# Optimization experiments

Measured on AMD Instinct MI355X. Metric: run time of the kernel, lower is better.

## Reference

```python
import jax, jax.numpy as jnp
import numpy as np

B, T, C = 4, 2048, 1024
H, D = 16, 64          # n_head, head_size; H*D == C
FF = 4 * C             # compute_layer_scaling * n_embed
EPS = 1e-5


def layernorm(x, g, b):
    mu = jnp.mean(x, axis=-1, keepdims=True)
    var = jnp.var(x, axis=-1, keepdims=True)
    return (x - mu) * jax.lax.rsqrt(var + EPS) * g + b


def setup_inputs() -> dict:
    key = jax.random.key(0)
    ks = jax.random.split(key, 12)
    s_c = 1.0 / np.sqrt(C)
    s_ff = 1.0 / np.sqrt(FF)
    return {
        "x": jax.random.normal(ks[0], (B, T, C), dtype=jnp.float32),
        # per-head Q/K/V weights, stacked: [H, C, D] (Linear with bias=False)
        "Wq": jax.random.normal(ks[1], (H, C, D), dtype=jnp.float32) * s_c,
        "Wk": jax.random.normal(ks[2], (H, C, D), dtype=jnp.float32) * s_c,
        "Wv": jax.random.normal(ks[3], (H, C, D), dtype=jnp.float32) * s_c,
        "Wproj": jax.random.normal(ks[4], (C, C), dtype=jnp.float32) * s_c,
        "bproj": jnp.zeros((C,), dtype=jnp.float32),
        "W1": jax.random.normal(ks[5], (C, FF), dtype=jnp.float32) * s_c,
        "b1": jnp.zeros((FF,), dtype=jnp.float32),
        "W2": jax.random.normal(ks[6], (FF, FF), dtype=jnp.float32) * s_ff,
        "b2": jnp.zeros((FF,), dtype=jnp.float32),
        "W3": jax.random.normal(ks[7], (FF, C), dtype=jnp.float32) * s_ff,
        "b3": jnp.zeros((C,), dtype=jnp.float32),
        "ln1_g": jnp.ones((C,), dtype=jnp.float32),
        "ln1_b": jnp.zeros((C,), dtype=jnp.float32),
        "ln2_g": jnp.ones((C,), dtype=jnp.float32),
        "ln2_b": jnp.zeros((C,), dtype=jnp.float32),
    }


def reference(x, Wq, Wk, Wv, Wproj, bproj, W1, b1, W2, b2, W3, b3,
              ln1_g, ln1_b, ln2_g, ln2_b):
    # --- multi-head causal self-attention (pre-LN) ---
    h = layernorm(x, ln1_g, ln1_b)
    q = jnp.einsum("btc,hcd->bhtd", h, Wq)
    k = jnp.einsum("btc,hcd->bhtd", h, Wk)
    v = jnp.einsum("btc,hcd->bhtd", h, Wv)
    # NOTE: original scales by n_embed**-0.5 (C from x.shape), not head_size
    scores = jnp.einsum("bhtd,bhsd->bhts", q, k) * (C ** -0.5)
    causal = jnp.tril(jnp.ones((T, T), dtype=bool))
    scores = jnp.where(causal, scores, -jnp.inf)
    wei = jax.nn.softmax(scores, axis=-1)          # dropout p=0 -> identity
    attn = jnp.einsum("bhts,bhsd->bhtd", wei, v)
    attn = attn.transpose(0, 2, 1, 3).reshape(B, T, C)  # concat heads
    x = x + attn @ Wproj + bproj
    # --- feed-forward (pre-LN): C -> FF -> relu -> FF -> relu -> C ---
    h2 = layernorm(x, ln2_g, ln2_b)
    h2 = jax.nn.relu(h2 @ W1 + b1)
    h2 = jax.nn.relu(h2 @ W2 + b2)
    x = x + h2 @ W3 + b3
    return x
```

## Files before the change

### kernel.cpp

```cpp
#include <hip/hip_runtime.h>

typedef __bf16 bf16;
typedef bf16  bf16x8 __attribute__((ext_vector_type(8)));
typedef bf16  bf16x4 __attribute__((ext_vector_type(4)));
typedef float f32x4  __attribute__((ext_vector_type(4)));

#define T_SEQ 2048

__device__ __forceinline__ void gload_lds16(const bf16* g, bf16* l) {
    __builtin_amdgcn_global_load_lds(
        (const __attribute__((address_space(1))) unsigned int*)g,
        (__attribute__((address_space(3))) unsigned int*)l,
        16, 0, 0);
}

#define VMCNT(n) asm volatile("s_waitcnt vmcnt(" #n ")" ::: "memory")
#define BAR() do { asm volatile("" ::: "memory"); __builtin_amdgcn_s_barrier(); \
                   asm volatile("" ::: "memory"); } while (0)

__global__ __launch_bounds__(256) void transpose_f32_bf16(
    const float* __restrict__ in, bf16* __restrict__ out, int R, int Cc, int ldo)
{
    __shared__ float tile[32][33];
    const int bx = blockIdx.x * 32;
    const int by = blockIdx.y * 32;
    const long bi = (long)blockIdx.z * R * Cc;
    const long bo = (long)blockIdx.z * Cc * ldo;
    const int tx = threadIdx.x, ty = threadIdx.y;
#pragma unroll
    for (int i = 0; i < 4; ++i)
        tile[ty + i * 8][tx] = in[bi + (long)(by + ty + i * 8) * Cc + bx + tx];
    __syncthreads();
#pragma unroll
    for (int i = 0; i < 4; ++i)
        out[bo + (long)(bx + ty + i * 8) * ldo + by + tx] = (bf16)tile[tx][ty + i * 8];
}

__global__ __launch_bounds__(256) void transpose_bf16(
    const bf16* __restrict__ in, bf16* __restrict__ out, int ldi, int ldo)
{
    __shared__ bf16 tile[32][33];
    const int bx = blockIdx.x * 32;
    const int by = blockIdx.y * 32;
    const int tx = threadIdx.x, ty = threadIdx.y;
#pragma unroll
    for (int i = 0; i < 4; ++i)
        tile[ty + i * 8][tx] = in[(long)(by + ty + i * 8) * ldi + bx + tx];
    __syncthreads();
#pragma unroll
    for (int i = 0; i < 4; ++i)
        out[(long)(bx + ty + i * 8) * ldo + by + tx] = tile[tx][ty + i * 8];
}

__global__ __launch_bounds__(256) void ln_kernel(
    const float* __restrict__ x, const float* __restrict__ g,
    const float* __restrict__ bb, bf16* __restrict__ out)
{
    const long row = blockIdx.x;
    const int tid = threadIdx.x;
    const float4 v = ((const float4*)(x + row * 1024))[tid];
    float s  = v.x + v.y + v.z + v.w;
    float s2 = v.x * v.x + v.y * v.y + v.z * v.z + v.w * v.w;
#pragma unroll
    for (int off = 32; off >= 1; off >>= 1) {
        s  += __shfl_xor(s,  off, 64);
        s2 += __shfl_xor(s2, off, 64);
    }
    __shared__ float red[8];
    const int wid = tid >> 6;
    if ((tid & 63) == 0) { red[wid] = s; red[4 + wid] = s2; }
    __syncthreads();
    s  = red[0] + red[1] + red[2] + red[3];
    s2 = red[4] + red[5] + red[6] + red[7];
    const float mu   = s * (1.f / 1024.f);
    const float rstd = rsqrtf(s2 * (1.f / 1024.f) - mu * mu + 1e-5f);
    const float4 gv = ((const float4*)g)[tid];
    const float4 bv = ((const float4*)bb)[tid];
    bf16x4 ov;
    ov[0] = (bf16)((v.x - mu) * rstd * gv.x + bv.x);
    ov[1] = (bf16)((v.y - mu) * rstd * gv.y + bv.y);
    ov[2] = (bf16)((v.z - mu) * rstd * gv.z + bv.z);
    ov[3] = (bf16)((v.w - mu) * rstd * gv.w + bv.w);
    *(bf16x4*)(out + row * 1024 + tid * 4) = ov;
}

#define LOADA(BUFP, QM) do {                                                   \
    const char* ab_ = (BUFP) + (size_t)((wr * 64 + (QM) * 128 + fr) * 128);    \
    _Pragma("unroll") for (int m_ = 0; m_ < 4; ++m_) {                         \
        af[m_][0] = *(const bf16x8*)(ab_ + m_ * 2048 + so0);                   \
        af[m_][1] = *(const bf16x8*)(ab_ + m_ * 2048 + so1); } } while (0)

#define LOADB(BUFP, QN, DST) do {                                              \
    const char* bb_ = (BUFP) + (size_t)((wc * 32 + (QN) * 128 + fr) * 128);    \
    _Pragma("unroll") for (int n_ = 0; n_ < 2; ++n_) {                         \
        DST[n_][0] = *(const bf16x8*)(bb_ + n_ * 2048 + so0);                  \
        DST[n_][1] = *(const bf16x8*)(bb_ + n_ * 2048 + so1); } } while (0)

#define MMA(ACC, BSET) do { __builtin_amdgcn_s_setprio(1);                     \
    _Pragma("unroll") for (int m_ = 0; m_ < 4; ++m_)                           \
    _Pragma("unroll") for (int n_ = 0; n_ < 2; ++n_) {                         \
        ACC[m_][n_] = __builtin_amdgcn_mfma_f32_16x16x32_bf16(                 \
            af[m_][0], BSET[n_][0], ACC[m_][n_], 0, 0, 0);                     \
        ACC[m_][n_] = __builtin_amdgcn_mfma_f32_16x16x32_bf16(                 \
            af[m_][1], BSET[n_][1], ACC[m_][n_], 0, 0, 0); }                   \
    __builtin_amdgcn_s_setprio(0); } while (0)

#define TB_DEEP(W1N, W3N, ISSN, ISSC) do {                                     \
    const char* abuf = cAs + ((size_t)cur << 15);                              \
    const char* bbuf = cBs + ((size_t)cur << 15);                              \
    const long kb  = (long)(k + 1) * 64;                                       \
    const long kb2 = (long)(k + 2) * 64;                                       \
    LOADA(abuf, 0);                                                            \
    LOADB(bbuf, 0, bfv0);                                                      \
    if (ISSN) stageB(nxt, 0, kb);                                 \
    BAR(); MMA(a00, bfv0); BAR();                                              \
    LOADB(bbuf, 1, bfv1);                                                      \
    if (ISSN) stageA(nxt, 1, kb);                                 \
    VMCNT(W1N);                                                                \
    BAR(); MMA(a01, bfv1); BAR();                                              \
    LOADA(abuf, 1);                                                            \
    if (ISSC) stageA(cur, 0, kb2);                                \
    BAR(); MMA(a11, bfv1); BAR();                                              \
    if (ISSC) stageB(cur, 1, kb2);                                \
    VMCNT(W3N);                                                                \
    BAR(); MMA(a10, bfv0); BAR(); } while (0)

template <int MODE>
__global__ __launch_bounds__(512, 1) void gemm256(
    const bf16* __restrict__ A, const bf16* __restrict__ Bt,
    const float* __restrict__ bias, const float* __restrict__ resid,
    void* __restrict__ outp, int M, int N, int K, int nbn)
{
    extern __shared__ __align__(16) char smem[];
    char* cAs = smem;
    char* cBs = smem + 65536;

    const int tid = threadIdx.x;
    const int wid = tid >> 6, lane = tid & 63;
    const int wr = wid >> 2, wc = wid & 3;
    const int fr = lane & 15, fq = lane >> 4;

    const int nwg = gridDim.x;
    const int cpx = nwg >> 3;
    const int b0  = blockIdx.x;
    const int bid = (b0 & 7) * cpx + (b0 >> 3);
    const long bm = bid / nbn, bn = bid % nbn;
    const long bmrow = bm * 256, bnrow = bn * 256;

    const int srow0 = wid * 8 + (lane >> 3);
    const int sslot = (lane & 7) ^ (lane >> 3);
    auto stageA = [&](int buf, int h, long kt) {
        const bf16* g = A + (size_t)(bmrow + h * 128 + srow0) * K + kt + sslot * 8;
        char* l = cAs + ((size_t)buf << 15) + h * 16384 + (size_t)wid * 1024;
        gload_lds16(g, (bf16*)l);
        gload_lds16(g + (size_t)64 * K, (bf16*)(l + 8192));
    };
    auto stageB = [&](int buf, int h, long kt) {
        const bf16* g = Bt + (size_t)(bnrow + h * 128 + srow0) * K + kt + sslot * 8;
        char* l = cBs + ((size_t)buf << 15) + h * 16384 + (size_t)wid * 1024;
        gload_lds16(g, (bf16*)l);
        gload_lds16(g + (size_t)64 * K, (bf16*)(l + 8192));
    };

    const int sx  = fr & 7;
    const int so0 = ((fq) ^ sx) * 16;
    const int so1 = ((4 + fq) ^ sx) * 16;

    bf16x8 af[4][2], bfv0[2][2], bfv1[2][2];
    f32x4 a00[4][2], a01[4][2], a11[4][2], a10[4][2];
#pragma unroll
    for (int m = 0; m < 4; ++m)
#pragma unroll
        for (int n = 0; n < 2; ++n) {
            a00[m][n] = {0.f, 0.f, 0.f, 0.f}; a01[m][n] = {0.f, 0.f, 0.f, 0.f};
            a11[m][n] = {0.f, 0.f, 0.f, 0.f}; a10[m][n] = {0.f, 0.f, 0.f, 0.f};
        }

    stageA(0, 0, 0);
    stageB(0, 1, 0);
    stageB(0, 0, 0);
    stageA(0, 1, 0);
    stageA(1, 0, 64);
    stageB(1, 1, 64);
    VMCNT(6);
    BAR();

    const int NT = K >> 6;
    int cur, nxt;
    int k = 0;
    for (; k < NT - 2; ++k) {
        cur = k & 1; nxt = cur ^ 1;
        TB_DEEP(8, 6, true, true);
    }
    cur = k & 1; nxt = cur ^ 1;
    TB_DEEP(8, 2, true, false);
    ++k;
    cur = k & 1; nxt = cur ^ 1;
    TB_DEEP(0, 0, false, false);

    auto writeQ = [&](f32x4 (&acc)[4][2], int QM, int QN) {
#pragma unroll
        for (int m = 0; m < 4; ++m) {
            const long row0 = bmrow + wr * 64 + QM * 128 + m * 16 + fq * 4;
#pragma unroll
            for (int n = 0; n < 2; ++n) {
                const long col = bnrow + wc * 32 + QN * 128 + n * 16 + fr;
                const float bv = (MODE == 0) ? 0.f : bias[col];
#pragma unroll
                for (int j = 0; j < 4; ++j) {
                    const long row = row0 + j;
                    float v = acc[m][n][j] + bv;
                    if (MODE == 1) v = fmaxf(v, 0.f);
                    if (MODE == 2) {
                        v += resid[row * N + col];
                        ((float*)outp)[row * N + col] = v;
                    } else {
                        ((bf16*)outp)[row * N + col] = (bf16)v;
                    }
                }
            }
        }
    };
    writeQ(a00, 0, 0); writeQ(a01, 0, 1); writeQ(a11, 1, 1); writeQ(a10, 1, 0);
}

#define TILE_BODY_N(PRE, LAST) do {                                            \
    const char* abuf = cAs + ((size_t)cur << 15);                              \
    const char* bbuf = cBs + ((size_t)cur << 14);                              \
    const long kn = (long)(k + 1) * 64;                                        \
    LOADA(abuf, 0);                                                            \
    LOADB(bbuf, 0, bfv);                                                       \
    if (PRE) { stageA(nxt, 0, kn); stageB(nxt, kn); stageA(nxt, 1, kn);        \
               VMCNT(6); }                                                     \
    else     { VMCNT(0); }                                                     \
    BAR(); MMA(aq0, bfv); BAR();                                               \
    LOADA(abuf, 1);                                                            \
    if (PRE) { VMCNT(2); }                                                     \
    if (!LAST) { BAR(); }                                                      \
    MMA(aq1, bfv);                                                             \
    if (!LAST) { BAR(); } } while (0)

template <int MODE>
__global__ __launch_bounds__(512, 2) void gemm256n(
    const bf16* __restrict__ A, const bf16* __restrict__ Bt,
    const float* __restrict__ bias, const float* __restrict__ resid,
    void* __restrict__ outp, int M, int N, int K, int nbn)
{
    extern __shared__ __align__(16) char smem[];
    char* cAs = smem;
    char* cBs = smem + 65536;

    const int tid = threadIdx.x;
    const int wid = tid >> 6, lane = tid & 63;
    const int wr = wid >> 2, wc = wid & 3;
    const int fr = lane & 15, fq = lane >> 4;

    const int nwg = gridDim.x;
    const int cpx = nwg >> 3;
    const int b0  = blockIdx.x;
    const int bid = (b0 & 7) * cpx + (b0 >> 3);
    const long bm = bid / nbn, bn = bid % nbn;
    const long bmrow = bm * 256, bnrow = bn * 128;

    const int srow0 = wid * 8 + (lane >> 3);
    const int sslot = (lane & 7) ^ (lane >> 3);
    auto stageA = [&](int buf, int h, long kt) {
        const bf16* g = A + (size_t)(bmrow + h * 128 + srow0) * K + kt + sslot * 8;
        char* l = cAs + ((size_t)buf << 15) + h * 16384 + (size_t)wid * 1024;
        gload_lds16(g, (bf16*)l);
        gload_lds16(g + (size_t)64 * K, (bf16*)(l + 8192));
    };
    auto stageB = [&](int buf, long kt) {
        const bf16* g = Bt + (size_t)(bnrow + srow0) * K + kt + sslot * 8;
        char* l = cBs + ((size_t)buf << 14) + (size_t)wid * 1024;
        gload_lds16(g, (bf16*)l);
        gload_lds16(g + (size_t)64 * K, (bf16*)(l + 8192));
    };

    const int sx  = fr & 7;
    const int so0 = ((fq) ^ sx) * 16;
    const int so1 = ((4 + fq) ^ sx) * 16;

    bf16x8 af[4][2], bfv[2][2];
    f32x4 aq0[4][2], aq1[4][2];
#pragma unroll
    for (int m = 0; m < 4; ++m)
#pragma unroll
        for (int n = 0; n < 2; ++n) {
            aq0[m][n] = {0.f, 0.f, 0.f, 0.f};
            aq1[m][n] = {0.f, 0.f, 0.f, 0.f};
        }

    stageA(0, 0, 0); stageB(0, 0); stageA(0, 1, 0);
    VMCNT(2);
    BAR();

    const int NT = K >> 6;
    int cur = 0, nxt = 1;
    int k = 0;
    for (; k < NT - 1; ++k) {
        cur = k & 1; nxt = cur ^ 1;
        TILE_BODY_N(true, false);
    }
    cur = k & 1; nxt = cur ^ 1;
    TILE_BODY_N(false, true);

    auto writeQ = [&](f32x4 (&acc)[4][2], int QM) {
#pragma unroll
        for (int m = 0; m < 4; ++m) {
            const long row0 = bmrow + wr * 64 + QM * 128 + m * 16 + fq * 4;
#pragma unroll
            for (int n = 0; n < 2; ++n) {
                const long col = bnrow + wc * 32 + n * 16 + fr;
                const float bv = (MODE == 0) ? 0.f : bias[col];
#pragma unroll
                for (int j = 0; j < 4; ++j) {
                    const long row = row0 + j;
                    float v = acc[m][n][j] + bv;
                    if (MODE == 1) v = fmaxf(v, 0.f);
                    if (MODE == 2) {
                        v += resid[row * N + col];
                        ((float*)outp)[row * N + col] = v;
                    } else {
                        ((bf16*)outp)[row * N + col] = (bf16)v;
                    }
                }
            }
        }
    };
    writeQ(aq0, 0); writeQ(aq1, 1);
}

__device__ __forceinline__ void attn_step(
    const bf16* __restrict__ Ks, const bf16* __restrict__ Vt,
    bf16* __restrict__ Pp, const bf16x8* qf,
    f32x4* o, f32x4& o_l, float* mj, const bf16x8 onesf,
    int fr, int fq, int qloc, bool diag)
{
    f32x4 s[4];
#pragma unroll
    for (int n = 0; n < 4; ++n) s[n] = {0.f, 0.f, 0.f, 0.f};
#pragma unroll
    for (int n = 0; n < 4; ++n) {
        const int t  = n * 16 + fr;
        const int sw = ((t ^ (t >> 3)) & 7) << 4;
#pragma unroll
        for (int kk = 0; kk < 2; ++kk) {
            const bf16x8 kf = *(const bf16x8*)((const char*)Ks + t * 128
                                               + ((kk * 64 + fq * 16) ^ sw));
            s[n] = __builtin_amdgcn_mfma_f32_16x16x32_bf16(qf[kk], kf, s[n], 0, 0, 0);
        }
    }
    float v[4][4], mxj[4];
#pragma unroll
    for (int j = 0; j < 4; ++j) {
        const int qg = qloc + fq * 4 + j;
        v[0][j] = s[0][j] * 0.03125f;
        v[1][j] = s[1][j] * 0.03125f;
        v[2][j] = s[2][j] * 0.03125f;
        v[3][j] = s[3][j] * 0.03125f;
        if (diag) {
            if (fr      > qg) v[0][j] = -1e30f;
            if (16 + fr > qg) v[1][j] = -1e30f;
            if (32 + fr > qg) v[2][j] = -1e30f;
            if (48 + fr > qg) v[3][j] = -1e30f;
        }
        float mx = fmaxf(fmaxf(v[0][j], v[1][j]), fmaxf(v[2][j], v[3][j]));
#pragma unroll
        for (int off = 1; off <= 8; off <<= 1) mx = fmaxf(mx, __shfl_xor(mx, off, 16));
        mxj[j] = mx;
    }
    float need = mxj[0] - mj[0];
    need = fmaxf(need, mxj[1] - mj[1]);
    need = fmaxf(need, mxj[2] - mj[2]);
    need = fmaxf(need, mxj[3] - mj[3]);
    if (__any(need > 8.f)) {
#pragma unroll
        for (int j = 0; j < 4; ++j) {
            const float mn   = fmaxf(mj[j], mxj[j]);
            const float corr = __expf(mj[j] - mn);
            mj[j] = mn;
#pragma unroll
            for (int nd = 0; nd < 4; ++nd) o[nd][j] *= corr;
            o_l[j] *= corr;
        }
    }
#pragma unroll
    for (int j = 0; j < 4; ++j) {
        bf16* prow = Pp + (fq * 4 + j) * 72;
        prow[fr]      = (bf16)__expf(v[0][j] - mj[j]);
        prow[16 + fr] = (bf16)__expf(v[1][j] - mj[j]);
        prow[32 + fr] = (bf16)__expf(v[2][j] - mj[j]);
        prow[48 + fr] = (bf16)__expf(v[3][j] - mj[j]);
    }
    asm volatile("s_waitcnt lgkmcnt(0)" ::: "memory");
    __builtin_amdgcn_sched_barrier(0);
    const bf16x8 pf0 = *(const bf16x8*)(Pp + fr * 72 + fq * 8);
    const bf16x8 pf1 = *(const bf16x8*)(Pp + fr * 72 + 32 + fq * 8);
#pragma unroll
    for (int nd = 0; nd < 4; ++nd) {
        const int dd = nd * 16 + fr;
        const int sw = ((dd ^ (dd >> 3)) & 7) << 4;
        const bf16x8 vf0 = *(const bf16x8*)((const char*)Vt + dd * 128 + ((fq * 16) ^ sw));
        const bf16x8 vf1 = *(const bf16x8*)((const char*)Vt + dd * 128 + ((64 + fq * 16) ^ sw));
        o[nd] = __builtin_amdgcn_mfma_f32_16x16x32_bf16(pf0, vf0, o[nd], 0, 0, 0);
        o[nd] = __builtin_amdgcn_mfma_f32_16x16x32_bf16(pf1, vf1, o[nd], 0, 0, 0);
    }
    o_l = __builtin_amdgcn_mfma_f32_16x16x32_bf16(pf0, onesf, o_l, 0, 0, 0);
    o_l = __builtin_amdgcn_mfma_f32_16x16x32_bf16(pf1, onesf, o_l, 0, 0, 0);
}

__global__ __launch_bounds__(256) void attn_kernel(
    const bf16* __restrict__ qkv, const bf16* __restrict__ vt,
    bf16* __restrict__ out)
{
    const int pair = blockIdx.x;
    const int h = blockIdx.y, b = blockIdx.z;
    const int tid = threadIdx.x, wid = tid >> 6, lane = tid & 63;
    const int fr = lane & 15, fq = lane >> 4;
    const int jA = pair, jB = 31 - pair;
    const bf16* baseQ = qkv + ((long)b * T_SEQ) * 3072 + h * 64;
    const bf16* baseK = baseQ + 1024;
    const bf16* baseV = vt + (long)(h * 64) * 8192 + (long)b * T_SEQ;

    __shared__ __align__(16) bf16 Ks[2][64 * 64];
    __shared__ __align__(16) bf16 Vs[2][64 * 64];
    __shared__ __align__(16) bf16 Plds[4][16 * 72];

    const int qrA = jA * 64 + wid * 16 + fr;
    const int qrB = jB * 64 + wid * 16 + fr;
    bf16x8 qfA[2], qfB[2];
#pragma unroll
    for (int kk = 0; kk < 2; ++kk) {
        qfA[kk] = *(const bf16x8*)(baseQ + (long)qrA * 3072 + kk * 32 + fq * 8);
        qfB[kk] = *(const bf16x8*)(baseQ + (long)qrB * 3072 + kk * 32 + fq * 8);
    }

    bf16x8 onesf;
    {
        const bf16 ov = (fr == 0) ? (bf16)1.f : (bf16)0.f;
#pragma unroll
        for (int e = 0; e < 8; ++e) onesf[e] = ov;
    }

    f32x4 oA[4], oB[4], olA, olB;
    float mA[4], mB[4];
#pragma unroll
    for (int nd = 0; nd < 4; ++nd) { oA[nd] = {0.f, 0.f, 0.f, 0.f}; oB[nd] = {0.f, 0.f, 0.f, 0.f}; }
    olA = {0.f, 0.f, 0.f, 0.f}; olB = {0.f, 0.f, 0.f, 0.f};
#pragma unroll
    for (int j = 0; j < 4; ++j) { mA[j] = -1e30f; mB[j] = -1e30f; }

    const int t_p0 = wid * 16 + (lane >> 3);
    const int t_p1 = t_p0 + 8;
    const int kcb0 = ((lane & 7) * 16) ^ (((t_p0 ^ (t_p0 >> 3)) & 7) << 4);
    const int kcb1 = ((lane & 7) * 16) ^ (((t_p1 ^ (t_p1 >> 3)) & 7) << 4);

    bf16* P = &Plds[wid][0];

    auto stage = [&](int buf, int c) {
        const long s0 = (long)c * 64;
        gload_lds16(baseK + (s0 + t_p0) * 3072 + (kcb0 >> 1), &Ks[buf][(wid * 2) * 512]);
        gload_lds16(baseK + (s0 + t_p1) * 3072 + (kcb1 >> 1), &Ks[buf][(wid * 2 + 1) * 512]);
        gload_lds16(baseV + (long)t_p0 * 8192 + s0 + (kcb0 >> 1), &Vs[buf][(wid * 2) * 512]);
        gload_lds16(baseV + (long)t_p1 * 8192 + s0 + (kcb1 >> 1), &Vs[buf][(wid * 2 + 1) * 512]);
    };

    const int nch = jB + 1;
    stage(0, 0);
    for (int c = 0; c < nch; ++c) {
        const int cur = c & 1;
        if (c + 1 < nch) { stage(cur ^ 1, c + 1); VMCNT(4); }
        else             { VMCNT(0); }
        BAR();
        if (c <= jA)
            attn_step(Ks[cur], Vs[cur], P, qfA, oA, olA, mA, onesf, fr, fq, wid * 16, c == jA);
        attn_step(Ks[cur], Vs[cur], P, qfB, oB, olB, mB, onesf, fr, fq, wid * 16, c == jB);
        BAR();
    }

#pragma unroll
    for (int j = 0; j < 4; ++j) {
        const float lA = __shfl(olA[j], lane & 48, 64);
        const float lB = __shfl(olB[j], lane & 48, 64);
        const float rA = 1.f / lA, rB = 1.f / lB;
        const long rowA = (long)b * T_SEQ + jA * 64 + wid * 16 + fq * 4 + j;
        const long rowB = (long)b * T_SEQ + jB * 64 + wid * 16 + fq * 4 + j;
#pragma unroll
        for (int nd = 0; nd < 4; ++nd) {
            out[rowA * 1024 + h * 64 + nd * 16 + fr] = (bf16)(oA[nd][j] * rA);
            out[rowB * 1024 + h * 64 + nd * 16 + fr] = (bf16)(oB[nd][j] * rB);
        }
    }
}

extern "C" void kernel_launch(void* const* d_in, const int* in_sizes, int n_in,
                              void* d_out, int out_size, void* d_ws, size_t ws_size,
                              hipStream_t stream)
{
    const float* x     = (const float*)d_in[0];
    const float* Wq    = (const float*)d_in[1];
    const float* Wk    = (const float*)d_in[2];
    const float* Wv    = (const float*)d_in[3];
    const float* Wproj = (const float*)d_in[4];
    const float* bproj = (const float*)d_in[5];
    const float* W1    = (const float*)d_in[6];
    const float* b1    = (const float*)d_in[7];
    const float* W2    = (const float*)d_in[8];
    const float* b2    = (const float*)d_in[9];
    const float* W3    = (const float*)d_in[10];
    const float* b3    = (const float*)d_in[11];
    const float* ln1g  = (const float*)d_in[12];
    const float* ln1b  = (const float*)d_in[13];
    const float* ln2g  = (const float*)d_in[14];
    const float* ln2b  = (const float*)d_in[15];

    char* ws = (char*)d_ws;
    size_t off = 0;
    auto alloc = [&](size_t bytes) {
        void* p = ws + off;
        off += (bytes + 255) & ~(size_t)255;
        return p;
    };
    bf16* Wqkv_t  = (bf16*)alloc(3072ul * 1024 * 2);
    bf16* Wproj_t = (bf16*)alloc(1024ul * 1024 * 2);
    bf16* W1_t    = (bf16*)alloc(4096ul * 1024 * 2);
    bf16* W2_t    = (bf16*)alloc(4096ul * 4096 * 2);
    bf16* W3_t    = (bf16*)alloc(1024ul * 4096 * 2);
    bf16* hbuf    = (bf16*)alloc(8192ul * 1024 * 2);
    float* x1     = (float*)alloc(8192ul * 1024 * 4);
    bf16* a1      = (bf16*)alloc(8192ul * 4096 * 2);
    char* R1      = (char*)alloc(8192ul * 4096 * 2);
    bf16* qkvb    = (bf16*)R1;
    bf16* attnb   = (bf16*)(R1 + 8192ul * 3072 * 2);
    bf16* a2      = (bf16*)R1;
    bf16* vt      = a1;

    hipFuncSetAttribute(reinterpret_cast<const void*>(&gemm256<1>),
                        hipFuncAttributeMaxDynamicSharedMemorySize, 131072);
    hipFuncSetAttribute(reinterpret_cast<const void*>(&gemm256n<0>),
                        hipFuncAttributeMaxDynamicSharedMemorySize, 98304);
    hipFuncSetAttribute(reinterpret_cast<const void*>(&gemm256n<2>),
                        hipFuncAttributeMaxDynamicSharedMemorySize, 98304);

    const dim3 tb(32, 8);
    transpose_f32_bf16<<<dim3(2, 32, 16), tb, 0, stream>>>(Wq, Wqkv_t,                1024, 64, 1024);
    transpose_f32_bf16<<<dim3(2, 32, 16), tb, 0, stream>>>(Wk, Wqkv_t + 1024l * 1024, 1024, 64, 1024);
    transpose_f32_bf16<<<dim3(2, 32, 16), tb, 0, stream>>>(Wv, Wqkv_t + 2048l * 1024, 1024, 64, 1024);
    transpose_f32_bf16<<<dim3(32, 32, 1),   tb, 0, stream>>>(Wproj, Wproj_t, 1024, 1024, 1024);
    transpose_f32_bf16<<<dim3(128, 32, 1),  tb, 0, stream>>>(W1, W1_t, 1024, 4096, 1024);
    transpose_f32_bf16<<<dim3(128, 128, 1), tb, 0, stream>>>(W2, W2_t, 4096, 4096, 4096);
    transpose_f32_bf16<<<dim3(32, 128, 1),  tb, 0, stream>>>(W3, W3_t, 4096, 1024, 4096);

    ln_kernel<<<8192, 256, 0, stream>>>(x, ln1g, ln1b, hbuf);
    gemm256n<0><<<768, 512, 98304, stream>>>(hbuf, Wqkv_t, nullptr, nullptr, qkvb,
                                             8192, 3072, 1024, 24);
    transpose_bf16<<<dim3(32, 256), tb, 0, stream>>>(qkvb + 2048, vt, 3072, 8192);
    attn_kernel<<<dim3(16, 16, 4), 256, 0, stream>>>(qkvb, vt, attnb);
    gemm256n<2><<<256, 512, 98304, stream>>>(attnb, Wproj_t, bproj, x, x1,
                                             8192, 1024, 1024, 8);
    ln_kernel<<<8192, 256, 0, stream>>>(x1, ln2g, ln2b, hbuf);
    gemm256<1><<<512, 512, 131072, stream>>>(hbuf, W1_t, b1, nullptr, a1,
                                             8192, 4096, 1024, 16);
    gemm256<1><<<512, 512, 131072, stream>>>(a1, W2_t, b2, nullptr, a2,
                                             8192, 4096, 4096, 16);
    gemm256n<2><<<256, 512, 98304, stream>>>(a2, W3_t, b3, x1, (float*)d_out,
                                             8192, 1024, 4096, 8);
}
```

Before: 677.5 us.

## Share K/V fragment loads across paired query tiles and store residual in bf16

The attention inner step now handles both query tiles (A and B) in one fused step. It loads each K and V fragment from LDS once and issues MFMAs for both tiles, using a separate P buffer per tile and raising wave priority around the MFMA blocks. The intermediate residual x1 is stored in bf16 instead of fp32, with a new bf16-input layernorm and new GEMM epilogue modes. This cuts LDS reads in attention and global traffic for the residual, at the cost of more register pressure and slightly lower residual precision.

```diff
diff --git a/kernel.cpp b/kernel.cpp
--- a/kernel.cpp
+++ b/kernel.cpp
@@ -81,6 +81,40 @@
     ov[1] = (bf16)((v.y - mu) * rstd * gv.y + bv.y);
     ov[2] = (bf16)((v.z - mu) * rstd * gv.z + bv.z);
     ov[3] = (bf16)((v.w - mu) * rstd * gv.w + bv.w);
+    *(bf16x4*)(out + row * 1024 + tid * 4) = ov;
+}
+
+__global__ __launch_bounds__(256) void ln_kernel_b(
+    const bf16* __restrict__ x, const float* __restrict__ g,
+    const float* __restrict__ bb, bf16* __restrict__ out)
+{
+    const long row = blockIdx.x;
+    const int tid = threadIdx.x;
+    const bf16x4 vb = ((const bf16x4*)(x + row * 1024))[tid];
+    const float v0 = (float)vb[0], v1 = (float)vb[1];
+    const float v2 = (float)vb[2], v3 = (float)vb[3];
+    float s  = v0 + v1 + v2 + v3;
+    float s2 = v0 * v0 + v1 * v1 + v2 * v2 + v3 * v3;
+#pragma unroll
+    for (int off = 32; off >= 1; off >>= 1) {
+        s  += __shfl_xor(s,  off, 64);
+        s2 += __shfl_xor(s2, off, 64);
+    }
+    __shared__ float red[8];
+    const int wid = tid >> 6;
+    if ((tid & 63) == 0) { red[wid] = s; red[4 + wid] = s2; }
+    __syncthreads();
+    s  = red[0] + red[1] + red[2] + red[3];
+    s2 = red[4] + red[5] + red[6] + red[7];
+    const float mu   = s * (1.f / 1024.f);
+    const float rstd = rsqrtf(s2 * (1.f / 1024.f) - mu * mu + 1e-5f);
+    const float4 gv = ((const float4*)g)[tid];
+    const float4 bv = ((const float4*)bb)[tid];
+    bf16x4 ov;
+    ov[0] = (bf16)((v0 - mu) * rstd * gv.x + bv.x);
+    ov[1] = (bf16)((v1 - mu) * rstd * gv.y + bv.y);
+    ov[2] = (bf16)((v2 - mu) * rstd * gv.z + bv.z);
+    ov[3] = (bf16)((v3 - mu) * rstd * gv.w + bv.w);
     *(bf16x4*)(out + row * 1024 + tid * 4) = ov;
 }
 
@@ -243,7 +277,7 @@
 template <int MODE>
 __global__ __launch_bounds__(512, 2) void gemm256n(
     const bf16* __restrict__ A, const bf16* __restrict__ Bt,
-    const float* __restrict__ bias, const float* __restrict__ resid,
+    const float* __restrict__ bias, const void* __restrict__ resid,
     void* __restrict__ outp, int M, int N, int K, int nbn)
 {
     extern __shared__ __align__(16) char smem[];
@@ -317,9 +351,11 @@
                 for (int j = 0; j < 4; ++j) {
                     const long row = row0 + j;
                     float v = acc[m][n][j] + bv;
-                    if (MODE == 1) v = fmaxf(v, 0.f);
-                    if (MODE == 2) {
-                        v += resid[row * N + col];
+                    if (MODE == 3) {
+                        v += ((const float*)resid)[row * N + col];
+                        ((bf16*)outp)[row * N + col] = (bf16)v;
+                    } else if (MODE == 4) {
+                        v += (float)((const bf16*)resid)[row * N + col];
                         ((float*)outp)[row * N + col] = v;
                     } else {
                         ((bf16*)outp)[row * N + col] = (bf16)v;
@@ -331,26 +367,10 @@
     writeQ(aq0, 0); writeQ(aq1, 1);
 }
 
-__device__ __forceinline__ void attn_step(
-    const bf16* __restrict__ Ks, const bf16* __restrict__ Vt,
-    bf16* __restrict__ Pp, const bf16x8* qf,
-    f32x4* o, f32x4& o_l, float* mj, const bf16x8 onesf,
+__device__ __forceinline__ void sm_part(
+    f32x4* s, float* mj, f32x4* o, f32x4& o_l, bf16* Pp,
     int fr, int fq, int qloc, bool diag)
 {
-    f32x4 s[4];
-#pragma unroll
-    for (int n = 0; n < 4; ++n) s[n] = {0.f, 0.f, 0.f, 0.f};
-#pragma unroll
-    for (int n = 0; n < 4; ++n) {
-        const int t  = n * 16 + fr;
-        const int sw = ((t ^ (t >> 3)) & 7) << 4;
-#pragma unroll
-        for (int kk = 0; kk < 2; ++kk) {
-            const bf16x8 kf = *(const bf16x8*)((const char*)Ks + t * 128
-                                               + ((kk * 64 + fq * 16) ^ sw));
-            s[n] = __builtin_amdgcn_mfma_f32_16x16x32_bf16(qf[kk], kf, s[n], 0, 0, 0);
-        }
-    }
     float v[4][4], mxj[4];
 #pragma unroll
     for (int j = 0; j < 4; ++j) {
@@ -370,10 +390,8 @@
         for (int off = 1; off <= 8; off <<= 1) mx = fmaxf(mx, __shfl_xor(mx, off, 16));
         mxj[j] = mx;
     }
-    float need = mxj[0] - mj[0];
-    need = fmaxf(need, mxj[1] - mj[1]);
-    need = fmaxf(need, mxj[2] - mj[2]);
-    need = fmaxf(need, mxj[3] - mj[3]);
+    float need = fmaxf(fmaxf(mxj[0] - mj[0], mxj[1] - mj[1]),
+                       fmaxf(mxj[2] - mj[2], mxj[3] - mj[3]));
     if (__any(need > 8.f)) {
 #pragma unroll
         for (int j = 0; j < 4; ++j) {
@@ -393,10 +411,34 @@
         prow[32 + fr] = (bf16)__expf(v[2][j] - mj[j]);
         prow[48 + fr] = (bf16)__expf(v[3][j] - mj[j]);
     }
+}
+
+__device__ __forceinline__ void attn_step(
+    const bf16* __restrict__ Ks, const bf16* __restrict__ Vt,
+    bf16* __restrict__ Pp, const bf16x8* qf,
+    f32x4* o, f32x4& o_l, float* mj, const bf16x8 onesf,
+    int fr, int fq, int qloc, bool diag)
+{
+    f32x4 s[4];
+#pragma unroll
+    for (int n = 0; n < 4; ++n) s[n] = {0.f, 0.f, 0.f, 0.f};
+    __builtin_amdgcn_s_setprio(1);
+#pragma unroll
+    for (int n = 0; n < 4; ++n) {
+        const int t  = n * 16 + fr;
+        const int sw = ((t ^ (t >> 3)) & 7) << 4;
+        const bf16x8 kf0 = *(const bf16x8*)((const char*)Ks + t * 128 + ((fq * 16) ^ sw));
+        const bf16x8 kf1 = *(const bf16x8*)((const char*)Ks + t * 128 + ((64 + fq * 16) ^ sw));
+        s[n] = __builtin_amdgcn_mfma_f32_16x16x32_bf16(qf[0], kf0, s[n], 0, 0, 0);
+        s[n] = __builtin_amdgcn_mfma_f32_16x16x32_bf16(qf[1], kf1, s[n], 0, 0, 0);
+    }
+    __builtin_amdgcn_s_setprio(0);
+    sm_part(s, mj, o, o_l, Pp, fr, fq, qloc, diag);
     asm volatile("s_waitcnt lgkmcnt(0)" ::: "memory");
     __builtin_amdgcn_sched_barrier(0);
     const bf16x8 pf0 = *(const bf16x8*)(Pp + fr * 72 + fq * 8);
     const bf16x8 pf1 = *(const bf16x8*)(Pp + fr * 72 + 32 + fq * 8);
+    __builtin_amdgcn_s_setprio(1);
 #pragma unroll
     for (int nd = 0; nd < 4; ++nd) {
         const int dd = nd * 16 + fr;
@@ -408,6 +450,58 @@
     }
     o_l = __builtin_amdgcn_mfma_f32_16x16x32_bf16(pf0, onesf, o_l, 0, 0, 0);
     o_l = __builtin_amdgcn_mfma_f32_16x16x32_bf16(pf1, onesf, o_l, 0, 0, 0);
+    __builtin_amdgcn_s_setprio(0);
+}
+
+__device__ __forceinline__ void attn_step2(
+    const bf16* __restrict__ Ks, const bf16* __restrict__ Vt,
+    bf16* __restrict__ PpA, bf16* __restrict__ PpB,
+    const bf16x8* qfA, const bf16x8* qfB,
+    f32x4* oA, f32x4& olA, float* mA,
+    f32x4* oB, f32x4& olB, float* mB,
+    const bf16x8 onesf, int fr, int fq, int qloc, bool diagA)
+{
+    f32x4 sA[4], sB[4];
+#pragma unroll
+    for (int n = 0; n < 4; ++n) { sA[n] = {0.f, 0.f, 0.f, 0.f}; sB[n] = {0.f, 0.f, 0.f, 0.f}; }
+    __builtin_amdgcn_s_setprio(1);
+#pragma unroll
+    for (int n = 0; n < 4; ++n) {
+        const int t  = n * 16 + fr;
+        const int sw = ((t ^ (t >> 3)) & 7) << 4;
+        const bf16x8 kf0 = *(const bf16x8*)((const char*)Ks + t * 128 + ((fq * 16) ^ sw));
+        const bf16x8 kf1 = *(const bf16x8*)((const char*)Ks + t * 128 + ((64 + fq * 16) ^ sw));
+        sA[n] = __builtin_amdgcn_mfma_f32_16x16x32_bf16(qfA[0], kf0, sA[n], 0, 0, 0);
+        sA[n] = __builtin_amdgcn_mfma_f32_16x16x32_bf16(qfA[1], kf1, sA[n], 0, 0, 0);
+        sB[n] = __builtin_amdgcn_mfma_f32_16x16x32_bf16(qfB[0], kf0, sB[n], 0, 0, 0);
+        sB[n] = __builtin_amdgcn_mfma_f32_16x16x32_bf16(qfB[1], kf1, sB[n], 0, 0, 0);
+    }
+    __builtin_amdgcn_s_setprio(0);
+    sm_part(sA, mA, oA, olA, PpA, fr, fq, qloc, diagA);
+    sm_part(sB, mB, oB, olB, PpB, fr, fq, qloc, false);
+    asm volatile("s_waitcnt lgkmcnt(0)" ::: "memory");
+    __builtin_amdgcn_sched_barrier(0);
+    const bf16x8 pfA0 = *(const bf16x8*)(PpA + fr * 72 + fq * 8);
+    const bf16x8 pfA1 = *(const bf16x8*)(PpA + fr * 72 + 32 + fq * 8);
+    const bf16x8 pfB0 = *(const bf16x8*)(PpB + fr * 72 + fq * 8);
+    const bf16x8 pfB1 = *(const bf16x8*)(PpB + fr * 72 + 32 + fq * 8);
+    __builtin_amdgcn_s_setprio(1);
+#pragma unroll
+    for (int nd = 0; nd < 4; ++nd) {
+        const int dd = nd * 16 + fr;
+        const int sw = ((dd ^ (dd >> 3)) & 7) << 4;
+        const bf16x8 vf0 = *(const bf16x8*)((const char*)Vt + dd * 128 + ((fq * 16) ^ sw));
+        const bf16x8 vf1 = *(const bf16x8*)((const char*)Vt + dd * 128 + ((64 + fq * 16) ^ sw));
+        oA[nd] = __builtin_amdgcn_mfma_f32_16x16x32_bf16(pfA0, vf0, oA[nd], 0, 0, 0);
+        oA[nd] = __builtin_amdgcn_mfma_f32_16x16x32_bf16(pfA1, vf1, oA[nd], 0, 0, 0);
+        oB[nd] = __builtin_amdgcn_mfma_f32_16x16x32_bf16(pfB0, vf0, oB[nd], 0, 0, 0);
+        oB[nd] = __builtin_amdgcn_mfma_f32_16x16x32_bf16(pfB1, vf1, oB[nd], 0, 0, 0);
+    }
+    olA = __builtin_amdgcn_mfma_f32_16x16x32_bf16(pfA0, onesf, olA, 0, 0, 0);
+    olA = __builtin_amdgcn_mfma_f32_16x16x32_bf16(pfA1, onesf, olA, 0, 0, 0);
+    olB = __builtin_amdgcn_mfma_f32_16x16x32_bf16(pfB0, onesf, olB, 0, 0, 0);
+    olB = __builtin_amdgcn_mfma_f32_16x16x32_bf16(pfB1, onesf, olB, 0, 0, 0);
+    __builtin_amdgcn_s_setprio(0);
 }
 
 __global__ __launch_bounds__(256) void attn_kernel(
@@ -425,7 +519,7 @@
 
     __shared__ __align__(16) bf16 Ks[2][64 * 64];
     __shared__ __align__(16) bf16 Vs[2][64 * 64];
-    __shared__ __align__(16) bf16 Plds[4][16 * 72];
+    __shared__ __align__(16) bf16 Plds[2][4][16 * 72];
 
     const int qrA = jA * 64 + wid * 16 + fr;
     const int qrB = jB * 64 + wid * 16 + fr;
@@ -456,7 +550,8 @@
     const int kcb0 = ((lane & 7) * 16) ^ (((t_p0 ^ (t_p0 >> 3)) & 7) << 4);
     const int kcb1 = ((lane & 7) * 16) ^ (((t_p1 ^ (t_p1 >> 3)) & 7) << 4);
 
-    bf16* P = &Plds[wid][0];
+    bf16* PA = &Plds[0][wid][0];
+    bf16* PB = &Plds[1][wid][0];
 
     auto stage = [&](int buf, int c) {
         const long s0 = (long)c * 64;
@@ -474,8 +569,11 @@
         else             { VMCNT(0); }
         BAR();
         if (c <= jA)
-            attn_step(Ks[cur], Vs[cur], P, qfA, oA, olA, mA, onesf, fr, fq, wid * 16, c == jA);
-        attn_step(Ks[cur], Vs[cur], P, qfB, oB, olB, mB, onesf, fr, fq, wid * 16, c == jB);
+            attn_step2(Ks[cur], Vs[cur], PA, PB, qfA, qfB,
+                       oA, olA, mA, oB, olB, mB, onesf, fr, fq, wid * 16, c == jA);
+        else
+            attn_step(Ks[cur], Vs[cur], PB, qfB, oB, olB, mB, onesf,
+                      fr, fq, wid * 16, c == jB);
         BAR();
     }
 
@@ -528,7 +626,7 @@
     bf16* W2_t    = (bf16*)alloc(4096ul * 4096 * 2);
     bf16* W3_t    = (bf16*)alloc(1024ul * 4096 * 2);
     bf16* hbuf    = (bf16*)alloc(8192ul * 1024 * 2);
-    float* x1     = (float*)alloc(8192ul * 1024 * 4);
+    bf16* x1b     = (bf16*)alloc(8192ul * 1024 * 2);
     bf16* a1      = (bf16*)alloc(8192ul * 4096 * 2);
     char* R1      = (char*)alloc(8192ul * 4096 * 2);
     bf16* qkvb    = (bf16*)R1;
@@ -540,7 +638,9 @@
                         hipFuncAttributeMaxDynamicSharedMemorySize, 131072);
     hipFuncSetAttribute(reinterpret_cast<const void*>(&gemm256n<0>),
                         hipFuncAttributeMaxDynamicSharedMemorySize, 98304);
-    hipFuncSetAttribute(reinterpret_cast<const void*>(&gemm256n<2>),
+    hipFuncSetAttribute(reinterpret_cast<const void*>(&gemm256n<3>),
+                        hipFuncAttributeMaxDynamicSharedMemorySize, 98304);
+    hipFuncSetAttribute(reinterpret_cast<const void*>(&gemm256n<4>),
                         hipFuncAttributeMaxDynamicSharedMemorySize, 98304);
 
     const dim3 tb(32, 8);
@@ -557,13 +657,13 @@
                                              8192, 3072, 1024, 24);
     transpose_bf16<<<dim3(32, 256), tb, 0, stream>>>(qkvb + 2048, vt, 3072, 8192);
     attn_kernel<<<dim3(16, 16, 4), 256, 0, stream>>>(qkvb, vt, attnb);
-    gemm256n<2><<<256, 512, 98304, stream>>>(attnb, Wproj_t, bproj, x, x1,
+    gemm256n<3><<<256, 512, 98304, stream>>>(attnb, Wproj_t, bproj, x, x1b,
                                              8192, 1024, 1024, 8);
-    ln_kernel<<<8192, 256, 0, stream>>>(x1, ln2g, ln2b, hbuf);
+    ln_kernel_b<<<8192, 256, 0, stream>>>(x1b, ln2g, ln2b, hbuf);
     gemm256<1><<<512, 512, 131072, stream>>>(hbuf, W1_t, b1, nullptr, a1,
                                              8192, 4096, 1024, 16);
     gemm256<1><<<512, 512, 131072, stream>>>(a1, W2_t, b2, nullptr, a2,
                                              8192, 4096, 4096, 16);
-    gemm256n<2><<<256, 512, 98304, stream>>>(a2, W3_t, b3, x1, (float*)d_out,
+    gemm256n<4><<<256, 512, 98304, stream>>>(a2, W3_t, b3, x1b, (float*)d_out,
                                              8192, 1024, 4096, 8);
 }
```

Result: no change. 665.5 us (median of 2 runs) (-1.8%).
